# Kernel tuning notes

Measured on AMD Instinct MI355X. Metric: run time of the kernel, lower is better.

## Reference

```python
import jax, jax.numpy as jnp
import numpy as np

NM = 50000   # member nodes
NP = 50000   # provider nodes
DM = 96      # member feature dim
DP = 128     # provider feature dim
IN_DIM = 128
HID = 256
LAT = 64
E = 1000000


def _sage_conv(x, src, dst, n, Wl, Wr, b):
    # PyG SAGEConv, mean aggregation: out = lin_l(mean_j x_j) + lin_r(x)
    msg = x[src]                                           # [E2, F]
    agg = jax.ops.segment_sum(msg, dst, num_segments=n)    # [N, F]
    deg = jax.ops.segment_sum(jnp.ones(src.shape[0], x.dtype), dst, num_segments=n)
    agg = agg / jnp.maximum(deg, 1.0)[:, None]
    return agg @ Wl.T + b + x @ Wr.T


def setup_inputs() -> dict:
    key = jax.random.key(0)
    ks = jax.random.split(key, 12)
    def g(k, shape, scale):
        return jax.random.normal(k, shape, jnp.float32) * scale
    inp = {
        "x_member": jax.random.normal(ks[0], (NM, DM), jnp.float32),
        "x_provider": jax.random.normal(ks[1], (NP, DP), jnp.float32),
        "edge_index": jnp.stack([
            jax.random.randint(ks[2], (E,), 0, NP),   # provider idx
            jax.random.randint(ks[3], (E,), 0, NM),   # member idx
        ], axis=0),
        # SAGEConv 1
        "W1l": g(ks[4], (HID, IN_DIM), (1.0 / IN_DIM) ** 0.5),
        "W1r": g(ks[5], (HID, IN_DIM), (1.0 / IN_DIM) ** 0.5),
        "b1": jnp.zeros((HID,), jnp.float32),
        # SAGEConv 2
        "W2l": g(ks[6], (LAT, HID), (1.0 / HID) ** 0.5),
        "W2r": g(ks[7], (LAT, HID), (1.0 / HID) ** 0.5),
        "b2": jnp.zeros((LAT,), jnp.float32),
        # decoder Linear(latent, in_dim)
        "Wd": g(ks[8], (IN_DIM, LAT), (1.0 / LAT) ** 0.5),
        "bd": jnp.zeros((IN_DIM,), jnp.float32),
    }
    return inp


def reference(x_member, x_provider, edge_index, W1l, W1r, b1, W2l, W2r, b2, Wd, bd):
    # pad member features to max_dim and concat (members first)
    xm = jnp.pad(x_member, ((0, 0), (0, IN_DIM - DM)))
    x = jnp.concatenate([xm, x_provider], axis=0)          # [NM+NP, IN_DIM]

    provider_idx = edge_index[0]
    member_idx = edge_index[1]
    # faithful to source: member indices are offset by NM in the combined graph
    src = jnp.concatenate([provider_idx, member_idx + NM])
    dst = jnp.concatenate([member_idx + NM, provider_idx])
    n = NM + NP

    h = jax.nn.relu(_sage_conv(x, src, dst, n, W1l, W1r, b1))
    # dropout: eval mode -> identity
    z = _sage_conv(h, src, dst, n, W2l, W2r, b2)            # [N, LAT]
    x_hat = z @ Wd.T + bd                                   # [N, IN_DIM]

    x_hat_member = x_hat[:NM]
    x_hat_provider = x_hat[NM:]
    member_z = z[:NM]
    provider_z = z[NM:]
    edge_logits = jnp.sum(provider_z[provider_idx] * member_z[member_idx], axis=1)
    return (x_hat_member, x_hat_provider, edge_logits)
```

## Files before the change

### kernel.cpp

```cpp
#include <hip/hip_runtime.h>
#include <stdint.h>

#define NMEM 50000
#define NTOT 100000
#define DMEM 96
#define DPRV 128
#define IND  128
#define HID  256
#define LATD 64
#define NEDGE 1000000

#define NB   196
#define VSH  9
#define NBV  512
#define EPB  4096

typedef __bf16 v8bf  __attribute__((ext_vector_type(8)));
typedef float  f32x4 __attribute__((ext_vector_type(4)));

__device__ __forceinline__ float bf2f(uint32_t u) {
    union { uint32_t u; float f; } x; x.u = u << 16; return x.f;
}
__device__ __forceinline__ uint32_t f2bf(float f) {
    union { float f; uint32_t u; } x; x.f = f;
    uint32_t r = x.u + 0x7fffu + ((x.u >> 16) & 1u);
    return r >> 16;
}
__device__ __forceinline__ int ld_ei(const int* ei, int idx, int i64) {
    return i64 ? ei[2 * idx] : ei[idx];
}

__global__ void k_detect(const uint16_t* __restrict__ w1l, const int* __restrict__ ei,
                         int* __restrict__ flags) {
    __shared__ int c1, c2;
    if (threadIdx.x == 0) { c1 = 0; c2 = 0; }
    __syncthreads();
    int big = 0;
    for (int i = threadIdx.x; i < 32768; i += 256) {
        float w = bf2f(w1l[i]);
        if (!(w > -2.0f && w < 2.0f)) big++;
    }
    int zhi = 0;
    for (int j = threadIdx.x; j < 2048; j += 256)
        if (ei[2 * j + 1] == 0) zhi++;
    atomicAdd(&c1, big);
    atomicAdd(&c2, zhi);
    __syncthreads();
    if (threadIdx.x == 0) {
        flags[0] = (c1 > 64) ? 1 : 0;
        flags[1] = (c2 > 1024) ? 1 : 0;
    }
}

__global__ void k_canon(const void* w1l, const void* w1r, const void* w2l,
                        const void* w2r, const void* wd, const void* b1,
                        const void* b2, const void* bd,
                        uint16_t* __restrict__ dstw, float* __restrict__ dstb,
                        const int* __restrict__ flags) {
    int g = blockIdx.x * 256 + threadIdx.x;
    int f32in = flags[0];
    if (g < 106496) {
        const void* src; int off;
        if (g < 65536) { int n = g >> 8, k = g & 255;
            src = (k < 128) ? w1l : w1r; off = n * 128 + (k & 127); }
        else if (g < 81920) { src = w2l; off = g - 65536; }
        else if (g < 98304) { src = w2r; off = g - 81920; }
        else                { src = wd;  off = g - 98304; }
        dstw[g] = f32in ? (uint16_t)f2bf(((const float*)src)[off])
                        : ((const uint16_t*)src)[off];
    } else if (g < 106944) {
        int o = g - 106496;
        const void* src; int off;
        if (o < 256)      { src = b1; off = o; }
        else if (o < 320) { src = b2; off = o - 256; }
        else              { src = bd; off = o - 320; }
        dstb[o] = f32in ? ((const float*)src)[off] : bf2f(((const uint16_t*)src)[off]);
    }
}

__global__ void k_build_x(const void* xm, const void* xp, uint16_t* __restrict__ Px,
                          uint16_t* __restrict__ Rx, const int* __restrict__ flags) {
    int idx = blockIdx.x * 256 + threadIdx.x;
    if (idx >= NTOT * 16) return;
    int v = idx >> 4, dblk = idx & 15;
    int d0 = dblk * 8;
    int f32in = flags[0];
    union { uint4 q; uint16_t u[8]; } o;
    if (v < NMEM) {
        if (d0 < DMEM) {
            if (f32in) {
                const float* s = (const float*)xm + (size_t)v * DMEM + d0;
                uint4 lo = *(const uint4*)s;
                uint4 hi = *(const uint4*)(s + 4);
                const float* lf = (const float*)&lo;
                const float* hf = (const float*)&hi;
#pragma unroll
                for (int i = 0; i < 4; i++) o.u[i] = (uint16_t)f2bf(lf[i]);
#pragma unroll
                for (int i = 0; i < 4; i++) o.u[4 + i] = (uint16_t)f2bf(hf[i]);
            } else {
                o.q = *(const uint4*)((const uint16_t*)xm + (size_t)v * DMEM + d0);
            }
        } else {
            o.q = (uint4){0, 0, 0, 0};
        }
    } else {
        int vv = v - NMEM;
        if (f32in) {
            const float* s = (const float*)xp + (size_t)vv * DPRV + d0;
            uint4 lo = *(const uint4*)s;
            uint4 hi = *(const uint4*)(s + 4);
            const float* lf = (const float*)&lo;
            const float* hf = (const float*)&hi;
#pragma unroll
            for (int i = 0; i < 4; i++) o.u[i] = (uint16_t)f2bf(lf[i]);
#pragma unroll
            for (int i = 0; i < 4; i++) o.u[4 + i] = (uint16_t)f2bf(hf[i]);
        } else {
            o.q = *(const uint4*)((const uint16_t*)xp + (size_t)vv * DPRV + d0);
        }
    }
    if (d0 < 64) *(uint4*)(Px + (size_t)v * 64 + d0) = o.q;
    else         *(uint4*)(Rx + (size_t)v * 64 + (d0 - 64)) = o.q;
}

__global__ __launch_bounds__(256) void k_pcount(const int* __restrict__ ei,
                                                int* __restrict__ bcount,
                                                const int* __restrict__ flags) {
    __shared__ int h[NB];
    int t = threadIdx.x;
    for (int i = t; i < NB; i += 256) h[i] = 0;
    __syncthreads();
    int i64 = flags[1];
    int j0 = blockIdx.x * EPB;
    int jend = min(j0 + EPB, NEDGE);
    for (int j = j0 + t; j < jend; j += 256) {
        int p = ld_ei(ei, j, i64), m = ld_ei(ei, NEDGE + j, i64);
        atomicAdd(&h[(NMEM + m) >> VSH], 1);
        atomicAdd(&h[p >> VSH], 1);
    }
    __syncthreads();
    for (int i = t; i < NB; i += 256) atomicAdd(&bcount[i], h[i]);
}

__global__ void k_bscan(const int* __restrict__ bcount, int* __restrict__ bbase,
                        int* __restrict__ bcursor, int* __restrict__ row_start) {
    __shared__ int s[256];
    int t = threadIdx.x;
    int v = (t < NB) ? bcount[t] : 0;
    s[t] = v; __syncthreads();
    for (int off = 1; off < 256; off <<= 1) {
        int x = (t >= off) ? s[t - off] : 0;
        __syncthreads();
        s[t] += x;
        __syncthreads();
    }
    if (t < NB) { bbase[t] = s[t] - v; bcursor[t] = s[t] - v; }
    if (t == 0) { bbase[NB] = 2 * NEDGE; row_start[NTOT] = 2 * NEDGE; }
}

__global__ __launch_bounds__(256) void k_part(const int* __restrict__ ei,
                                              int* __restrict__ bcursor,
                                              uint32_t* __restrict__ part,
                                              const int* __restrict__ flags) {
    __shared__ int h[NB], gb[NB], cur[NB];
    int t = threadIdx.x;
    for (int i = t; i < NB; i += 256) { h[i] = 0; cur[i] = 0; }
    __syncthreads();
    int i64 = flags[1];
    int j0 = blockIdx.x * EPB;
    int jend = min(j0 + EPB, NEDGE);
    for (int j = j0 + t; j < jend; j += 256) {
        int p = ld_ei(ei, j, i64), m = ld_ei(ei, NEDGE + j, i64);
        atomicAdd(&h[(NMEM + m) >> VSH], 1);
        atomicAdd(&h[p >> VSH], 1);
    }
    __syncthreads();
    for (int i = t; i < NB; i += 256) gb[i] = atomicAdd(&bcursor[i], h[i]);
    __syncthreads();
    for (int j = j0 + t; j < jend; j += 256) {
        int p = ld_ei(ei, j, i64), m = ld_ei(ei, NEDGE + j, i64);
        int d1 = NMEM + m;
        int d2 = p;
        int b1 = d1 >> VSH, b2 = d2 >> VSH;
        int r1 = atomicAdd(&cur[b1], 1);
        part[gb[b1] + r1] = ((uint32_t)(d1 & (NBV - 1)) << 17) | (uint32_t)p;
        int r2 = atomicAdd(&cur[b2], 1);
        part[gb[b2] + r2] = ((uint32_t)(d2 & (NBV - 1)) << 17) | (uint32_t)(NMEM + m);
    }
}

__global__ __launch_bounds__(256) void k_sort(const uint32_t* __restrict__ part,
                                              const int* __restrict__ bbase,
                                              int* __restrict__ row_start,
                                              int* __restrict__ colg) {
    __shared__ int sa[NBV], sb[NBV];
    int k = blockIdx.x, t = threadIdx.x;
    int base = bbase[k];
    int cnt  = bbase[k + 1] - base;
    for (int i = t; i < NBV; i += 256) sa[i] = 0;
    __syncthreads();
    for (int i = t; i < cnt; i += 256) {
        uint32_t e = part[base + i];
        atomicAdd(&sa[e >> 17], 1);
    }
    __syncthreads();
    int* src = sa; int* dst = sb;
    for (int off = 1; off < NBV; off <<= 1) {
        for (int i = t; i < NBV; i += 256)
            dst[i] = src[i] + (i >= off ? src[i - off] : 0);
        __syncthreads();
        int* tmp = src; src = dst; dst = tmp;
    }
    for (int i = t; i < NBV; i += 256) {
        int excl = (i > 0) ? src[i - 1] : 0;
        dst[i] = excl;
        int gv = (k << VSH) + i;
        if (gv < NTOT) row_start[gv] = base + excl;
    }
    __syncthreads();
    for (int i = t; i < cnt; i += 256) {
        uint32_t e = part[base + i];
        int dloc = (int)(e >> 17);
        int pos = atomicAdd(&dst[dloc], 1);
        colg[base + pos] = (int)(e & 0x1FFFFu);
    }
}

__global__ __launch_bounds__(256) void k_agg1(const uint16_t* __restrict__ Px,
                                              const uint16_t* __restrict__ Rx,
                                              const int* __restrict__ row_start,
                                              const int* __restrict__ colg,
                                              uint16_t* __restrict__ A1) {
    int t = threadIdx.x;
    int half = (t & 63) >> 5;
    int v = blockIdx.x * 8 + (t >> 6) * 2 + half;
    int l32 = t & 31;
    int slot = l32 >> 4, cg = l32 & 15;
    const uint16_t* base = (cg < 8) ? Px : Rx;
    int co = (cg & 7) * 8;
    int start = row_start[v], end = row_start[v + 1];
    float a0[8] = {0.f, 0.f, 0.f, 0.f, 0.f, 0.f, 0.f, 0.f};
    float a1[8] = {0.f, 0.f, 0.f, 0.f, 0.f, 0.f, 0.f, 0.f};
    int b = start + slot;
    for (; b + 2 < end; b += 4) {
        int s0 = colg[b], s1 = colg[b + 2];
        union { uint4 q; uint16_t u[8]; } f0, f1;
        f0.q = *(const uint4*)(base + (size_t)s0 * 64 + co);
        f1.q = *(const uint4*)(base + (size_t)s1 * 64 + co);
#pragma unroll
        for (int i = 0; i < 8; i++) { a0[i] += bf2f(f0.u[i]); a1[i] += bf2f(f1.u[i]); }
    }
    if (b < end) {
        int s0 = colg[b];
        union { uint4 q; uint16_t u[8]; } f0;
        f0.q = *(const uint4*)(base + (size_t)s0 * 64 + co);
#pragma unroll
        for (int i = 0; i < 8; i++) a0[i] += bf2f(f0.u[i]);
    }
#pragma unroll
    for (int i = 0; i < 8; i++) {
        a0[i] += a1[i];
        a0[i] += __shfl_xor(a0[i], 16);
    }
    if (slot == 0) {
        float inv = 1.0f / (float)max(end - start, 1);
        union { uint4 q; uint16_t u[8]; } o;
#pragma unroll
        for (int i = 0; i < 8; i++) o.u[i] = (uint16_t)f2bf(a0[i] * inv);
        *(uint4*)(A1 + (size_t)v * 128 + cg * 8) = o.q;
    }
}

__global__ __launch_bounds__(256, 4) void k_gemm1(const uint16_t* __restrict__ A1,
                                                  const uint16_t* __restrict__ canonb,
                                                  const float* __restrict__ biasf,
                                                  uint16_t* __restrict__ P,
                                                  uint16_t* __restrict__ R) {
    __shared__ uint16_t As[64][264];
    int t = threadIdx.x;
    int w = t >> 6, lane = t & 63;
    int m16 = lane & 15, q = lane >> 4;
    int row0 = blockIdx.x * 64;

    uint4 stg[8];
#pragma unroll
    for (int i = 0; i < 8; i++) {
        int c = t + i * 256;
        int row = c >> 5, seg = c & 31;
        int grow = min(row0 + row, NTOT - 1);
        int k0 = seg * 8;
        const uint16_t* src;
        if (k0 < 128)      src = A1 + (size_t)grow * 128 + k0;
        else if (k0 < 192) src = P + (size_t)grow * 64 + (k0 - 128);
        else               src = R + (size_t)grow * 64 + (k0 - 192);
        stg[i] = *(const uint4*)src;
    }
#pragma unroll
    for (int i = 0; i < 8; i++) {
        int c = t + i * 256;
        *(uint4*)&As[c >> 5][(c & 31) * 8] = stg[i];
    }
    __syncthreads();

    uint32_t hpk[4][4][2];
#pragma unroll
    for (int pn = 0; pn < 4; pn++) {
        int col = w * 64 + pn * 16 + m16;
        v8bf b1[8];
#pragma unroll
        for (int ks = 0; ks < 8; ks++)
            b1[ks] = *(const v8bf*)(canonb + (size_t)col * 256 + ks * 32 + q * 8);
        f32x4 acc[4];
#pragma unroll
        for (int mt = 0; mt < 4; mt++) acc[mt] = (f32x4){0.f, 0.f, 0.f, 0.f};
#pragma unroll
        for (int mt = 0; mt < 4; mt++) {
#pragma unroll
            for (int ks = 0; ks < 8; ks++) {
                v8bf a = *(const v8bf*)&As[mt * 16 + m16][ks * 32 + q * 8];
                acc[mt] = __builtin_amdgcn_mfma_f32_16x16x32_bf16(b1[ks], a, acc[mt], 0, 0, 0);
            }
        }
        int cb = w * 64 + pn * 16 + q * 4;
        f32x4 bb = *(const f32x4*)&biasf[cb];
#pragma unroll
        for (int mt = 0; mt < 4; mt++) {
            float v0 = fmaxf(acc[mt][0] + bb[0], 0.f);
            float v1 = fmaxf(acc[mt][1] + bb[1], 0.f);
            float v2 = fmaxf(acc[mt][2] + bb[2], 0.f);
            float v3 = fmaxf(acc[mt][3] + bb[3], 0.f);
            hpk[pn][mt][0] = f2bf(v0) | (f2bf(v1) << 16);
            hpk[pn][mt][1] = f2bf(v2) | (f2bf(v3) << 16);
        }
        __builtin_amdgcn_sched_barrier(0);
    }
    __syncthreads();

#pragma unroll
    for (int pn = 0; pn < 4; pn++) {
        int cb = w * 64 + pn * 16 + q * 4;
#pragma unroll
        for (int mt = 0; mt < 4; mt++) {
            uint2 v; v.x = hpk[pn][mt][0]; v.y = hpk[pn][mt][1];
            *(uint2*)&As[mt * 16 + m16][cb] = v;
        }
    }
    __syncthreads();

    v8bf b2[2][8];
#pragma unroll
    for (int n = 0; n < 2; n++) {
        int c2 = w * 32 + n * 16 + m16;
        const uint16_t* s2 = canonb + (c2 < 64 ? (65536 + c2 * 256) : (81920 + (c2 - 64) * 256));
#pragma unroll
        for (int ks = 0; ks < 8; ks++)
            b2[n][ks] = *(const v8bf*)(s2 + ks * 32 + q * 8);
    }
    f32x4 acc2[4][2];
#pragma unroll
    for (int mt = 0; mt < 4; mt++) {
        acc2[mt][0] = (f32x4){0.f, 0.f, 0.f, 0.f};
        acc2[mt][1] = (f32x4){0.f, 0.f, 0.f, 0.f};
    }
#pragma unroll
    for (int mt = 0; mt < 4; mt++) {
#pragma unroll
        for (int ks = 0; ks < 8; ks++) {
            v8bf hf = *(const v8bf*)&As[mt * 16 + m16][ks * 32 + q * 8];
            acc2[mt][0] = __builtin_amdgcn_mfma_f32_16x16x32_bf16(b2[0][ks], hf, acc2[mt][0], 0, 0, 0);
            acc2[mt][1] = __builtin_amdgcn_mfma_f32_16x16x32_bf16(b2[1][ks], hf, acc2[mt][1], 0, 0, 0);
        }
    }
#pragma unroll
    for (int n = 0; n < 2; n++) {
        int cb = w * 32 + n * 16 + q * 4;
        int isR = cb >= 64;
        int cl = cb - (isR ? 64 : 0);
        f32x4 bb;
        if (isR) bb = *(const f32x4*)&biasf[256 + cl];
        else     bb = (f32x4){0.f, 0.f, 0.f, 0.f};
        uint16_t* dst = isR ? R : P;
#pragma unroll
        for (int mt = 0; mt < 4; mt++) {
            int row = row0 + mt * 16 + m16;
            if (row < NTOT) {
                uint2 v;
                v.x = f2bf(acc2[mt][n][0] + bb[0]) | (f2bf(acc2[mt][n][1] + bb[1]) << 16);
                v.y = f2bf(acc2[mt][n][2] + bb[2]) | (f2bf(acc2[mt][n][3] + bb[3]) << 16);
                *(uint2*)(dst + (size_t)row * 64 + cl) = v;
            }
        }
    }
}

__global__ __launch_bounds__(256) void k_agg2z(const uint16_t* __restrict__ P,
                                               const uint16_t* __restrict__ R,
                                               const int* __restrict__ row_start,
                                               const int* __restrict__ colg,
                                               uint16_t* __restrict__ Z) {
    int t = threadIdx.x;
    int half = (t & 63) >> 5;
    int v = blockIdx.x * 8 + (t >> 6) * 2 + half;
    int l32 = t & 31;
    int slot = l32 >> 3, cg = l32 & 7;
    int start = row_start[v], end = row_start[v + 1];
    float a0[8] = {0.f, 0.f, 0.f, 0.f, 0.f, 0.f, 0.f, 0.f};
    float a1[8] = {0.f, 0.f, 0.f, 0.f, 0.f, 0.f, 0.f, 0.f};
    int b = start + slot;
    for (; b + 4 < end; b += 8) {
        int s0 = colg[b], s1 = colg[b + 4];
        union { uint4 q; uint16_t u[8]; } f0, f1;
        f0.q = *(const uint4*)(P + (size_t)s0 * 64 + cg * 8);
        f1.q = *(const uint4*)(P + (size_t)s1 * 64 + cg * 8);
#pragma unroll
        for (int i = 0; i < 8; i++) { a0[i] += bf2f(f0.u[i]); a1[i] += bf2f(f1.u[i]); }
    }
    if (b < end) {
        int s0 = colg[b];
        union { uint4 q; uint16_t u[8]; } f0;
        f0.q = *(const uint4*)(P + (size_t)s0 * 64 + cg * 8);
#pragma unroll
        for (int i = 0; i < 8; i++) a0[i] += bf2f(f0.u[i]);
    }
#pragma unroll
    for (int i = 0; i < 8; i++) {
        a0[i] += a1[i];
        a0[i] += __shfl_xor(a0[i], 8);
        a0[i] += __shfl_xor(a0[i], 16);
    }
    if (slot == 0) {
        float inv = 1.0f / (float)max(end - start, 1);
        union { uint4 q; uint16_t u[8]; } rr, o;
        rr.q = *(const uint4*)(R + (size_t)v * 64 + cg * 8);
#pragma unroll
        for (int i = 0; i < 8; i++)
            o.u[i] = (uint16_t)f2bf(a0[i] * inv + bf2f(rr.u[i]));
        *(uint4*)(Z + (size_t)v * 64 + cg * 8) = o.q;
    }
}

__global__ __launch_bounds__(256, 2) void k_gemm3(const uint16_t* __restrict__ Z,
                                                  const uint16_t* __restrict__ canonb,
                                                  const float* __restrict__ biasf,
                                                  float* __restrict__ outf) {
    int wave = threadIdx.x >> 6, lane = threadIdx.x & 63;
    int m16 = lane & 15, quad = lane >> 4;
    int row0 = (blockIdx.x * 4 + wave) * 16;
    int arow = min(row0 + m16, NTOT - 1);
    v8bf a0 = *(const v8bf*)(Z + (size_t)arow * 64 + quad * 8);
    v8bf a1 = *(const v8bf*)(Z + (size_t)arow * 64 + 32 + quad * 8);
    v8bf b0[8], b1[8];
#pragma unroll
    for (int nt = 0; nt < 8; nt++) {
        b0[nt] = *(const v8bf*)(canonb + 98304 + (size_t)(nt * 16 + m16) * 64 + quad * 8);
        b1[nt] = *(const v8bf*)(canonb + 98304 + (size_t)(nt * 16 + m16) * 64 + 32 + quad * 8);
    }
    f32x4 acc[8];
#pragma unroll
    for (int i = 0; i < 8; i++) acc[i] = (f32x4){0.f, 0.f, 0.f, 0.f};
#pragma unroll
    for (int nt = 0; nt < 8; nt++) {
        acc[nt] = __builtin_amdgcn_mfma_f32_16x16x32_bf16(a0, b0[nt], acc[nt], 0, 0, 0);
        acc[nt] = __builtin_amdgcn_mfma_f32_16x16x32_bf16(a1, b1[nt], acc[nt], 0, 0, 0);
    }
#pragma unroll
    for (int nt = 0; nt < 8; nt++) {
        int col = nt * 16 + m16;
        float bia = biasf[320 + col];
#pragma unroll
        for (int r = 0; r < 4; r++) {
            int row = row0 + quad * 4 + r;
            if (row < NTOT) outf[(size_t)row * 128 + col] = acc[nt][r] + bia;
        }
    }
}

__global__ __launch_bounds__(256) void k_logits(const int* __restrict__ ei,
                                                const uint16_t* __restrict__ Z,
                                                float* __restrict__ out,
                                                const int* __restrict__ flags) {
    int t = blockIdx.x * 256 + threadIdx.x;
    int j = t >> 3, sub = t & 7;
    if (j >= NEDGE) return;
    int i64 = flags[1];
    int p = ld_ei(ei, j, i64), m = ld_ei(ei, NEDGE + j, i64);
    union { uint4 q; uint16_t u[8]; } a, b;
    a.q = *(const uint4*)(Z + (size_t)(NMEM + p) * 64 + sub * 8);
    b.q = *(const uint4*)(Z + (size_t)m * 64 + sub * 8);
    float d = 0.f;
#pragma unroll
    for (int i = 0; i < 8; i++) d += bf2f(a.u[i]) * bf2f(b.u[i]);
    d += __shfl_xor(d, 1);
    d += __shfl_xor(d, 2);
    d += __shfl_xor(d, 4);
    if (sub == 0) out[j] = d;
}

__global__ void k_zero_out(float* __restrict__ out, int n4) {
    int i = blockIdx.x * 256 + threadIdx.x;
    if (i < n4) ((uint4*)out)[i] = (uint4){0, 0, 0, 0};
}
__global__ void k_sentinel(float* __restrict__ out, const int* __restrict__ flags,
                           int ws_mb) {
    if (blockIdx.x == 0 && threadIdx.x == 0)
        out[0] = 1000.0f + (float)ws_mb + 4096.0f * flags[0] + 8192.0f * flags[1];
}

extern "C" void kernel_launch(void* const* d_in, const int* in_sizes, int n_in,
                              void* d_out, int out_size, void* d_ws, size_t ws_size,
                              hipStream_t stream) {
    const void* xm = d_in[0];
    const void* xp = d_in[1];
    const int*  ei = (const int*)d_in[2];
    float* outf = (float*)d_out;

    const size_t NEED = 73019648;
    if (ws_size < NEED) {
        int* flags = (int*)d_ws;
        k_detect<<<1, 256, 0, stream>>>((const uint16_t*)d_in[3], ei, flags);
        int n4 = out_size / 4;
        k_zero_out<<<(n4 + 255) / 256, 256, 0, stream>>>(outf, n4);
        k_sentinel<<<1, 64, 0, stream>>>(outf, flags, (int)(ws_size >> 20));
        return;
    }

    char* ws = (char*)d_ws;
    int* colg       = (int*)(ws + 0);
    int* bmeta      = (int*)(ws + 8000000);
    int* bucket_count  = bmeta;
    int* bucket_base   = bmeta + 256;
    int* bucket_cursor = bmeta + 512;
    int* row_start  = (int*)(ws + 8400384);
    int* flags      = (int*)(ws + 8800768) + 100;
    uint16_t* canonb= (uint16_t*)(ws + 8804864);
    float* biasf    = (float*)(ws + 9017856);
    uint16_t* A1    = (uint16_t*)(ws + 9019648);
    uint32_t* part  = (uint32_t*)A1;
    uint16_t* P     = (uint16_t*)(ws + 34619648);
    uint16_t* R     = (uint16_t*)(ws + 47419648);
    uint16_t* Z     = (uint16_t*)(ws + 60219648);

    const int PGRID = (NEDGE + EPB - 1) / EPB;

    k_detect<<<1, 256, 0, stream>>>((const uint16_t*)d_in[3], ei, flags);
    k_canon<<<418, 256, 0, stream>>>(d_in[3], d_in[4], d_in[6], d_in[7], d_in[9],
                                     d_in[5], d_in[8], d_in[10], canonb, biasf, flags);
    k_build_x<<<(NTOT * 16 + 255) / 256, 256, 0, stream>>>(xm, xp, P, R, flags);
    hipMemsetAsync(bucket_count, 0, 256 * sizeof(int), stream);
    k_pcount<<<PGRID, 256, 0, stream>>>(ei, bucket_count, flags);
    k_bscan<<<1, 256, 0, stream>>>(bucket_count, bucket_base, bucket_cursor, row_start);
    k_part<<<PGRID, 256, 0, stream>>>(ei, bucket_cursor, part, flags);
    k_sort<<<NB, 256, 0, stream>>>(part, bucket_base, row_start, colg);
    k_agg1<<<NTOT / 8, 256, 0, stream>>>(P, R, row_start, colg, A1);
    k_gemm1<<<(NTOT + 63) / 64, 256, 0, stream>>>(A1, canonb, biasf, P, R);
    k_agg2z<<<NTOT / 8, 256, 0, stream>>>(P, R, row_start, colg, Z);
    k_gemm3<<<1563, 256, 0, stream>>>(Z, canonb, biasf, outf);
    k_logits<<<NEDGE * 8 / 256, 256, 0, stream>>>(ei, Z, outf + 12800000, flags);
}
```

Baseline: 400.4 us.

## Fuse layer-1 neighbor mean aggregation into the GEMM1 kernel prologue

Removes the separate k_agg1 kernel and computes the mean-aggregated neighbor features directly into GEMM1's shared-memory A tile, so the A1 intermediate is never written to or read from global memory. GEMM1 now writes its outputs to separate Pn/Rn buffers instead of overwriting its inputs in place, because other blocks still gather from the old features. The cost is that each 256-thread GEMM block now runs the irregular gather itself, 8 rows per wave, with only 1563 blocks at limited occupancy. That may expose gather latency that k_agg1's 12500 small blocks used to hide.

```diff
diff --git a/kernel.cpp b/kernel.cpp
--- a/kernel.cpp
+++ b/kernel.cpp
@@ -227,79 +227,72 @@
     }
 }
 
-__global__ __launch_bounds__(256) void k_agg1(const uint16_t* __restrict__ Px,
-                                              const uint16_t* __restrict__ Rx,
-                                              const int* __restrict__ row_start,
-                                              const int* __restrict__ colg,
-                                              uint16_t* __restrict__ A1) {
-    int t = threadIdx.x;
-    int half = (t & 63) >> 5;
-    int v = blockIdx.x * 8 + (t >> 6) * 2 + half;
-    int l32 = t & 31;
-    int slot = l32 >> 4, cg = l32 & 15;
-    const uint16_t* base = (cg < 8) ? Px : Rx;
-    int co = (cg & 7) * 8;
-    int start = row_start[v], end = row_start[v + 1];
-    float a0[8] = {0.f, 0.f, 0.f, 0.f, 0.f, 0.f, 0.f, 0.f};
-    float a1[8] = {0.f, 0.f, 0.f, 0.f, 0.f, 0.f, 0.f, 0.f};
-    int b = start + slot;
-    for (; b + 2 < end; b += 4) {
-        int s0 = colg[b], s1 = colg[b + 2];
-        union { uint4 q; uint16_t u[8]; } f0, f1;
-        f0.q = *(const uint4*)(base + (size_t)s0 * 64 + co);
-        f1.q = *(const uint4*)(base + (size_t)s1 * 64 + co);
-#pragma unroll
-        for (int i = 0; i < 8; i++) { a0[i] += bf2f(f0.u[i]); a1[i] += bf2f(f1.u[i]); }
-    }
-    if (b < end) {
-        int s0 = colg[b];
-        union { uint4 q; uint16_t u[8]; } f0;
-        f0.q = *(const uint4*)(base + (size_t)s0 * 64 + co);
-#pragma unroll
-        for (int i = 0; i < 8; i++) a0[i] += bf2f(f0.u[i]);
-    }
-#pragma unroll
-    for (int i = 0; i < 8; i++) {
-        a0[i] += a1[i];
-        a0[i] += __shfl_xor(a0[i], 16);
-    }
-    if (slot == 0) {
-        float inv = 1.0f / (float)max(end - start, 1);
-        union { uint4 q; uint16_t u[8]; } o;
-#pragma unroll
-        for (int i = 0; i < 8; i++) o.u[i] = (uint16_t)f2bf(a0[i] * inv);
-        *(uint4*)(A1 + (size_t)v * 128 + cg * 8) = o.q;
-    }
-}
-
-__global__ __launch_bounds__(256, 4) void k_gemm1(const uint16_t* __restrict__ A1,
+__global__ __launch_bounds__(256, 4) void k_gemm1(const uint16_t* __restrict__ Px,
+                                                  const uint16_t* __restrict__ Rx,
+                                                  const int* __restrict__ row_start,
+                                                  const int* __restrict__ colg,
                                                   const uint16_t* __restrict__ canonb,
                                                   const float* __restrict__ biasf,
-                                                  uint16_t* __restrict__ P,
-                                                  uint16_t* __restrict__ R) {
+                                                  uint16_t* __restrict__ Pn,
+                                                  uint16_t* __restrict__ Rn) {
     __shared__ uint16_t As[64][264];
     int t = threadIdx.x;
     int w = t >> 6, lane = t & 63;
     int m16 = lane & 15, q = lane >> 4;
     int row0 = blockIdx.x * 64;
 
-    uint4 stg[8];
-#pragma unroll
-    for (int i = 0; i < 8; i++) {
+#pragma unroll
+    for (int i = 0; i < 4; i++) {
         int c = t + i * 256;
-        int row = c >> 5, seg = c & 31;
+        int row = c >> 4, seg = c & 15;
         int grow = min(row0 + row, NTOT - 1);
-        int k0 = seg * 8;
-        const uint16_t* src;
-        if (k0 < 128)      src = A1 + (size_t)grow * 128 + k0;
-        else if (k0 < 192) src = P + (size_t)grow * 64 + (k0 - 128);
-        else               src = R + (size_t)grow * 64 + (k0 - 192);
-        stg[i] = *(const uint4*)src;
-    }
-#pragma unroll
-    for (int i = 0; i < 8; i++) {
-        int c = t + i * 256;
-        *(uint4*)&As[c >> 5][(c & 31) * 8] = stg[i];
+        int k0 = 128 + seg * 8;
+        const uint16_t* src = (k0 < 192) ? (Px + (size_t)grow * 64 + (k0 - 128))
+                                         : (Rx + (size_t)grow * 64 + (k0 - 192));
+        *(uint4*)&As[row][k0] = *(const uint4*)src;
+    }
+
+    {
+        int half = lane >> 5;
+        int l32 = lane & 31;
+        int slot = l32 >> 4, cg = l32 & 15;
+        const uint16_t* gb = (cg < 8) ? Px : Rx;
+        int co = (cg & 7) * 8;
+        for (int vv = 0; vv < 8; vv++) {
+            int r = w * 16 + vv * 2 + half;
+            int v = min(row0 + r, NTOT - 1);
+            int start = row_start[v], end = row_start[v + 1];
+            float a0[8] = {0.f, 0.f, 0.f, 0.f, 0.f, 0.f, 0.f, 0.f};
+            float a1[8] = {0.f, 0.f, 0.f, 0.f, 0.f, 0.f, 0.f, 0.f};
+            int b = start + slot;
+            for (; b + 2 < end; b += 4) {
+                int s0 = colg[b], s1 = colg[b + 2];
+                union { uint4 q; uint16_t u[8]; } f0, f1;
+                f0.q = *(const uint4*)(gb + (size_t)s0 * 64 + co);
+                f1.q = *(const uint4*)(gb + (size_t)s1 * 64 + co);
+#pragma unroll
+                for (int i = 0; i < 8; i++) { a0[i] += bf2f(f0.u[i]); a1[i] += bf2f(f1.u[i]); }
+            }
+            if (b < end) {
+                int s0 = colg[b];
+                union { uint4 q; uint16_t u[8]; } f0;
+                f0.q = *(const uint4*)(gb + (size_t)s0 * 64 + co);
+#pragma unroll
+                for (int i = 0; i < 8; i++) a0[i] += bf2f(f0.u[i]);
+            }
+#pragma unroll
+            for (int i = 0; i < 8; i++) {
+                a0[i] += a1[i];
+                a0[i] += __shfl_xor(a0[i], 16);
+            }
+            if (slot == 0) {
+                float inv = 1.0f / (float)max(end - start, 1);
+                union { uint4 q; uint16_t u[8]; } o;
+#pragma unroll
+                for (int i = 0; i < 8; i++) o.u[i] = (uint16_t)f2bf(a0[i] * inv);
+                *(uint4*)&As[r][cg * 8] = o.q;
+            }
+        }
     }
     __syncthreads();
 
@@ -380,7 +373,7 @@
         f32x4 bb;
         if (isR) bb = *(const f32x4*)&biasf[256 + cl];
         else     bb = (f32x4){0.f, 0.f, 0.f, 0.f};
-        uint16_t* dst = isR ? R : P;
+        uint16_t* dst = isR ? Rn : Pn;
 #pragma unroll
         for (int mt = 0; mt < 4; mt++) {
             int row = row0 + mt * 16 + m16;
@@ -535,10 +528,11 @@
     int* flags      = (int*)(ws + 8800768) + 100;
     uint16_t* canonb= (uint16_t*)(ws + 8804864);
     float* biasf    = (float*)(ws + 9017856);
-    uint16_t* A1    = (uint16_t*)(ws + 9019648);
-    uint32_t* part  = (uint32_t*)A1;
-    uint16_t* P     = (uint16_t*)(ws + 34619648);
-    uint16_t* R     = (uint16_t*)(ws + 47419648);
+    uint16_t* Pn    = (uint16_t*)(ws + 9019648);
+    uint16_t* Rn    = (uint16_t*)(ws + 21819648);
+    uint32_t* part  = (uint32_t*)Pn;
+    uint16_t* Px    = (uint16_t*)(ws + 34619648);
+    uint16_t* Rx    = (uint16_t*)(ws + 47419648);
     uint16_t* Z     = (uint16_t*)(ws + 60219648);
 
     const int PGRID = (NEDGE + EPB - 1) / EPB;
@@ -546,15 +540,15 @@
     k_detect<<<1, 256, 0, stream>>>((const uint16_t*)d_in[3], ei, flags);
     k_canon<<<418, 256, 0, stream>>>(d_in[3], d_in[4], d_in[6], d_in[7], d_in[9],
                                      d_in[5], d_in[8], d_in[10], canonb, biasf, flags);
-    k_build_x<<<(NTOT * 16 + 255) / 256, 256, 0, stream>>>(xm, xp, P, R, flags);
+    k_build_x<<<(NTOT * 16 + 255) / 256, 256, 0, stream>>>(xm, xp, Px, Rx, flags);
     hipMemsetAsync(bucket_count, 0, 256 * sizeof(int), stream);
     k_pcount<<<PGRID, 256, 0, stream>>>(ei, bucket_count, flags);
     k_bscan<<<1, 256, 0, stream>>>(bucket_count, bucket_base, bucket_cursor, row_start);
     k_part<<<PGRID, 256, 0, stream>>>(ei, bucket_cursor, part, flags);
     k_sort<<<NB, 256, 0, stream>>>(part, bucket_base, row_start, colg);
-    k_agg1<<<NTOT / 8, 256, 0, stream>>>(P, R, row_start, colg, A1);
-    k_gemm1<<<(NTOT + 63) / 64, 256, 0, stream>>>(A1, canonb, biasf, P, R);
-    k_agg2z<<<NTOT / 8, 256, 0, stream>>>(P, R, row_start, colg, Z);
+    k_gemm1<<<(NTOT + 63) / 64, 256, 0, stream>>>(Px, Rx, row_start, colg,
+                                                  canonb, biasf, Pn, Rn);
+    k_agg2z<<<NTOT / 8, 256, 0, stream>>>(Pn, Rn, row_start, colg, Z);
     k_gemm3<<<1563, 256, 0, stream>>>(Z, canonb, biasf, outf);
     k_logits<<<NEDGE * 8 / 256, 256, 0, stream>>>(ei, Z, outf + 12800000, flags);
 }
```

Result: slower. 424.6 us (+6.1%).

## Merge prep kernels, merge output kernels, skip zero-padded member columns in agg1

Applied to the files above, without the earlier changes.

The weight canonicalisation, feature build and partition count kernels become one launch (k_prep), with block ranges picking the role. The decoder GEMM and edge-logit kernels are also merged into one launch (k_out). In agg1, lanes that gather the padded-zero feature columns 96..127 for provider-destination rows skip their loads, since those source rows are members whose padding is zero. The aim is fewer launches and less gather traffic, at the cost of mixed-role blocks with different register and occupancy needs.

```diff
diff --git a/kernel.cpp b/kernel.cpp
--- a/kernel.cpp
+++ b/kernel.cpp
@@ -15,6 +15,10 @@
 #define NBV  512
 #define EPB  4096
 
+#define PREP_PCOUNT 245
+#define PREP_CANON  418
+#define G3B 1563
+
 typedef __bf16 v8bf  __attribute__((ext_vector_type(8)));
 typedef float  f32x4 __attribute__((ext_vector_type(4)));
 
@@ -52,39 +56,62 @@
     }
 }
 
-__global__ void k_canon(const void* w1l, const void* w1r, const void* w2l,
-                        const void* w2r, const void* wd, const void* b1,
-                        const void* b2, const void* bd,
-                        uint16_t* __restrict__ dstw, float* __restrict__ dstb,
-                        const int* __restrict__ flags) {
-    int g = blockIdx.x * 256 + threadIdx.x;
+__global__ __launch_bounds__(256) void k_prep(const void* w1l, const void* w1r,
+                                              const void* w2l, const void* w2r,
+                                              const void* wd, const void* b1,
+                                              const void* b2, const void* bd,
+                                              const void* xm, const void* xp,
+                                              const int* __restrict__ ei,
+                                              uint16_t* __restrict__ dstw,
+                                              float* __restrict__ dstb,
+                                              uint16_t* __restrict__ Px,
+                                              uint16_t* __restrict__ Rx,
+                                              int* __restrict__ bcount,
+                                              const int* __restrict__ flags) {
+    __shared__ int h[NB];
+    int bid = blockIdx.x;
+    int t = threadIdx.x;
     int f32in = flags[0];
-    if (g < 106496) {
-        const void* src; int off;
-        if (g < 65536) { int n = g >> 8, k = g & 255;
-            src = (k < 128) ? w1l : w1r; off = n * 128 + (k & 127); }
-        else if (g < 81920) { src = w2l; off = g - 65536; }
-        else if (g < 98304) { src = w2r; off = g - 81920; }
-        else                { src = wd;  off = g - 98304; }
-        dstw[g] = f32in ? (uint16_t)f2bf(((const float*)src)[off])
-                        : ((const uint16_t*)src)[off];
-    } else if (g < 106944) {
-        int o = g - 106496;
-        const void* src; int off;
-        if (o < 256)      { src = b1; off = o; }
-        else if (o < 320) { src = b2; off = o - 256; }
-        else              { src = bd; off = o - 320; }
-        dstb[o] = f32in ? ((const float*)src)[off] : bf2f(((const uint16_t*)src)[off]);
-    }
-}
-
-__global__ void k_build_x(const void* xm, const void* xp, uint16_t* __restrict__ Px,
-                          uint16_t* __restrict__ Rx, const int* __restrict__ flags) {
-    int idx = blockIdx.x * 256 + threadIdx.x;
+    if (bid < PREP_PCOUNT) {
+        for (int i = t; i < NB; i += 256) h[i] = 0;
+        __syncthreads();
+        int i64 = flags[1];
+        int j0 = bid * EPB;
+        int jend = min(j0 + EPB, NEDGE);
+        for (int j = j0 + t; j < jend; j += 256) {
+            int p = ld_ei(ei, j, i64), m = ld_ei(ei, NEDGE + j, i64);
+            atomicAdd(&h[(NMEM + m) >> VSH], 1);
+            atomicAdd(&h[p >> VSH], 1);
+        }
+        __syncthreads();
+        for (int i = t; i < NB; i += 256) atomicAdd(&bcount[i], h[i]);
+        return;
+    }
+    if (bid < PREP_PCOUNT + PREP_CANON) {
+        int g = (bid - PREP_PCOUNT) * 256 + t;
+        if (g < 106496) {
+            const void* src; int off;
+            if (g < 65536) { int n = g >> 8, k = g & 255;
+                src = (k < 128) ? w1l : w1r; off = n * 128 + (k & 127); }
+            else if (g < 81920) { src = w2l; off = g - 65536; }
+            else if (g < 98304) { src = w2r; off = g - 81920; }
+            else                { src = wd;  off = g - 98304; }
+            dstw[g] = f32in ? (uint16_t)f2bf(((const float*)src)[off])
+                            : ((const uint16_t*)src)[off];
+        } else if (g < 106944) {
+            int o = g - 106496;
+            const void* src; int off;
+            if (o < 256)      { src = b1; off = o; }
+            else if (o < 320) { src = b2; off = o - 256; }
+            else              { src = bd; off = o - 320; }
+            dstb[o] = f32in ? ((const float*)src)[off] : bf2f(((const uint16_t*)src)[off]);
+        }
+        return;
+    }
+    int idx = (bid - PREP_PCOUNT - PREP_CANON) * 256 + t;
     if (idx >= NTOT * 16) return;
     int v = idx >> 4, dblk = idx & 15;
     int d0 = dblk * 8;
-    int f32in = flags[0];
     union { uint4 q; uint16_t u[8]; } o;
     if (v < NMEM) {
         if (d0 < DMEM) {
@@ -122,25 +149,6 @@
     }
     if (d0 < 64) *(uint4*)(Px + (size_t)v * 64 + d0) = o.q;
     else         *(uint4*)(Rx + (size_t)v * 64 + (d0 - 64)) = o.q;
-}
-
-__global__ __launch_bounds__(256) void k_pcount(const int* __restrict__ ei,
-                                                int* __restrict__ bcount,
-                                                const int* __restrict__ flags) {
-    __shared__ int h[NB];
-    int t = threadIdx.x;
-    for (int i = t; i < NB; i += 256) h[i] = 0;
-    __syncthreads();
-    int i64 = flags[1];
-    int j0 = blockIdx.x * EPB;
-    int jend = min(j0 + EPB, NEDGE);
-    for (int j = j0 + t; j < jend; j += 256) {
-        int p = ld_ei(ei, j, i64), m = ld_ei(ei, NEDGE + j, i64);
-        atomicAdd(&h[(NMEM + m) >> VSH], 1);
-        atomicAdd(&h[p >> VSH], 1);
-    }
-    __syncthreads();
-    for (int i = t; i < NB; i += 256) atomicAdd(&bcount[i], h[i]);
 }
 
 __global__ void k_bscan(const int* __restrict__ bcount, int* __restrict__ bbase,
@@ -242,21 +250,24 @@
     int start = row_start[v], end = row_start[v + 1];
     float a0[8] = {0.f, 0.f, 0.f, 0.f, 0.f, 0.f, 0.f, 0.f};
     float a1[8] = {0.f, 0.f, 0.f, 0.f, 0.f, 0.f, 0.f, 0.f};
-    int b = start + slot;
-    for (; b + 2 < end; b += 4) {
-        int s0 = colg[b], s1 = colg[b + 2];
-        union { uint4 q; uint16_t u[8]; } f0, f1;
-        f0.q = *(const uint4*)(base + (size_t)s0 * 64 + co);
-        f1.q = *(const uint4*)(base + (size_t)s1 * 64 + co);
-#pragma unroll
-        for (int i = 0; i < 8; i++) { a0[i] += bf2f(f0.u[i]); a1[i] += bf2f(f1.u[i]); }
-    }
-    if (b < end) {
-        int s0 = colg[b];
-        union { uint4 q; uint16_t u[8]; } f0;
-        f0.q = *(const uint4*)(base + (size_t)s0 * 64 + co);
-#pragma unroll
-        for (int i = 0; i < 8; i++) a0[i] += bf2f(f0.u[i]);
+    bool skip = (v >= NMEM) && (cg >= 12);
+    if (!skip) {
+        int b = start + slot;
+        for (; b + 2 < end; b += 4) {
+            int s0 = colg[b], s1 = colg[b + 2];
+            union { uint4 q; uint16_t u[8]; } f0, f1;
+            f0.q = *(const uint4*)(base + (size_t)s0 * 64 + co);
+            f1.q = *(const uint4*)(base + (size_t)s1 * 64 + co);
+#pragma unroll
+            for (int i = 0; i < 8; i++) { a0[i] += bf2f(f0.u[i]); a1[i] += bf2f(f1.u[i]); }
+        }
+        if (b < end) {
+            int s0 = colg[b];
+            union { uint4 q; uint16_t u[8]; } f0;
+            f0.q = *(const uint4*)(base + (size_t)s0 * 64 + co);
+#pragma unroll
+            for (int i = 0; i < 8; i++) a0[i] += bf2f(f0.u[i]);
+        }
     }
 #pragma unroll
     for (int i = 0; i < 8; i++) {
@@ -440,47 +451,47 @@
     }
 }
 
-__global__ __launch_bounds__(256, 2) void k_gemm3(const uint16_t* __restrict__ Z,
-                                                  const uint16_t* __restrict__ canonb,
-                                                  const float* __restrict__ biasf,
-                                                  float* __restrict__ outf) {
-    int wave = threadIdx.x >> 6, lane = threadIdx.x & 63;
-    int m16 = lane & 15, quad = lane >> 4;
-    int row0 = (blockIdx.x * 4 + wave) * 16;
-    int arow = min(row0 + m16, NTOT - 1);
-    v8bf a0 = *(const v8bf*)(Z + (size_t)arow * 64 + quad * 8);
-    v8bf a1 = *(const v8bf*)(Z + (size_t)arow * 64 + 32 + quad * 8);
-    v8bf b0[8], b1[8];
-#pragma unroll
-    for (int nt = 0; nt < 8; nt++) {
-        b0[nt] = *(const v8bf*)(canonb + 98304 + (size_t)(nt * 16 + m16) * 64 + quad * 8);
-        b1[nt] = *(const v8bf*)(canonb + 98304 + (size_t)(nt * 16 + m16) * 64 + 32 + quad * 8);
-    }
-    f32x4 acc[8];
-#pragma unroll
-    for (int i = 0; i < 8; i++) acc[i] = (f32x4){0.f, 0.f, 0.f, 0.f};
-#pragma unroll
-    for (int nt = 0; nt < 8; nt++) {
-        acc[nt] = __builtin_amdgcn_mfma_f32_16x16x32_bf16(a0, b0[nt], acc[nt], 0, 0, 0);
-        acc[nt] = __builtin_amdgcn_mfma_f32_16x16x32_bf16(a1, b1[nt], acc[nt], 0, 0, 0);
-    }
-#pragma unroll
-    for (int nt = 0; nt < 8; nt++) {
-        int col = nt * 16 + m16;
-        float bia = biasf[320 + col];
-#pragma unroll
-        for (int r = 0; r < 4; r++) {
-            int row = row0 + quad * 4 + r;
-            if (row < NTOT) outf[(size_t)row * 128 + col] = acc[nt][r] + bia;
-        }
-    }
-}
-
-__global__ __launch_bounds__(256) void k_logits(const int* __restrict__ ei,
+__global__ __launch_bounds__(256, 4) void k_out(const int* __restrict__ ei,
                                                 const uint16_t* __restrict__ Z,
-                                                float* __restrict__ out,
+                                                const uint16_t* __restrict__ canonb,
+                                                const float* __restrict__ biasf,
+                                                float* __restrict__ outf,
                                                 const int* __restrict__ flags) {
-    int t = blockIdx.x * 256 + threadIdx.x;
+    int bid = blockIdx.x;
+    if (bid < G3B) {
+        int wave = threadIdx.x >> 6, lane = threadIdx.x & 63;
+        int m16 = lane & 15, quad = lane >> 4;
+        int row0 = (bid * 4 + wave) * 16;
+        int arow = min(row0 + m16, NTOT - 1);
+        v8bf a0 = *(const v8bf*)(Z + (size_t)arow * 64 + quad * 8);
+        v8bf a1 = *(const v8bf*)(Z + (size_t)arow * 64 + 32 + quad * 8);
+        v8bf b0[8], b1[8];
+#pragma unroll
+        for (int nt = 0; nt < 8; nt++) {
+            b0[nt] = *(const v8bf*)(canonb + 98304 + (size_t)(nt * 16 + m16) * 64 + quad * 8);
+            b1[nt] = *(const v8bf*)(canonb + 98304 + (size_t)(nt * 16 + m16) * 64 + 32 + quad * 8);
+        }
+        f32x4 acc[8];
+#pragma unroll
+        for (int i = 0; i < 8; i++) acc[i] = (f32x4){0.f, 0.f, 0.f, 0.f};
+#pragma unroll
+        for (int nt = 0; nt < 8; nt++) {
+            acc[nt] = __builtin_amdgcn_mfma_f32_16x16x32_bf16(a0, b0[nt], acc[nt], 0, 0, 0);
+            acc[nt] = __builtin_amdgcn_mfma_f32_16x16x32_bf16(a1, b1[nt], acc[nt], 0, 0, 0);
+        }
+#pragma unroll
+        for (int nt = 0; nt < 8; nt++) {
+            int col = nt * 16 + m16;
+            float bia = biasf[320 + col];
+#pragma unroll
+            for (int r = 0; r < 4; r++) {
+                int row = row0 + quad * 4 + r;
+                if (row < NTOT) outf[(size_t)row * 128 + col] = acc[nt][r] + bia;
+            }
+        }
+        return;
+    }
+    int t = (bid - G3B) * 256 + threadIdx.x;
     int j = t >> 3, sub = t & 7;
     if (j >= NEDGE) return;
     int i64 = flags[1];
@@ -494,7 +505,7 @@
     d += __shfl_xor(d, 1);
     d += __shfl_xor(d, 2);
     d += __shfl_xor(d, 4);
-    if (sub == 0) out[j] = d;
+    if (sub == 0) outf[12800000 + j] = d;
 }
 
 __global__ void k_zero_out(float* __restrict__ out, int n4) {
@@ -541,20 +552,16 @@
     uint16_t* R     = (uint16_t*)(ws + 47419648);
     uint16_t* Z     = (uint16_t*)(ws + 60219648);
 
-    const int PGRID = (NEDGE + EPB - 1) / EPB;
-
     k_detect<<<1, 256, 0, stream>>>((const uint16_t*)d_in[3], ei, flags);
-    k_canon<<<418, 256, 0, stream>>>(d_in[3], d_in[4], d_in[6], d_in[7], d_in[9],
-                                     d_in[5], d_in[8], d_in[10], canonb, biasf, flags);
-    k_build_x<<<(NTOT * 16 + 255) / 256, 256, 0, stream>>>(xm, xp, P, R, flags);
     hipMemsetAsync(bucket_count, 0, 256 * sizeof(int), stream);
-    k_pcount<<<PGRID, 256, 0, stream>>>(ei, bucket_count, flags);
+    k_prep<<<PREP_PCOUNT + PREP_CANON + (NTOT * 16 + 255) / 256, 256, 0, stream>>>(
+        d_in[3], d_in[4], d_in[6], d_in[7], d_in[9], d_in[5], d_in[8], d_in[10],
+        xm, xp, ei, canonb, biasf, P, R, bucket_count, flags);
     k_bscan<<<1, 256, 0, stream>>>(bucket_count, bucket_base, bucket_cursor, row_start);
-    k_part<<<PGRID, 256, 0, stream>>>(ei, bucket_cursor, part, flags);
+    k_part<<<PREP_PCOUNT, 256, 0, stream>>>(ei, bucket_cursor, part, flags);
     k_sort<<<NB, 256, 0, stream>>>(part, bucket_base, row_start, colg);
     k_agg1<<<NTOT / 8, 256, 0, stream>>>(P, R, row_start, colg, A1);
     k_gemm1<<<(NTOT + 63) / 64, 256, 0, stream>>>(A1, canonb, biasf, P, R);
     k_agg2z<<<NTOT / 8, 256, 0, stream>>>(P, R, row_start, colg, Z);
-    k_gemm3<<<1563, 256, 0, stream>>>(Z, canonb, biasf, outf);
-    k_logits<<<NEDGE * 8 / 256, 256, 0, stream>>>(ei, Z, outf + 12800000, flags);
-}
+    k_out<<<G3B + NEDGE * 8 / 256, 256, 0, stream>>>(ei, Z, canonb, biasf, outf, flags);
+}
```

New measurement: 391.4 us. 2.2% less time.
